# Kernel tuning notes

Measured on AMD Instinct MI355X. Metric: run time of the kernel, lower is better.

## Reference

```python
import jax, jax.numpy as jnp
import numpy as np

N_NODES = 50000
N_EDGES = 800000
HIDDEN = 64
NUM_FEATURES = 1
OUT_DIM = 2


def setup_inputs() -> dict:
    key = jax.random.key(0)
    k = jax.random.split(key, 6)
    x = jax.random.normal(k[0], (N_NODES, NUM_FEATURES), dtype=jnp.float32)
    edge_index = jax.random.randint(k[1], (2, N_EDGES), 0, N_NODES, dtype=jnp.int32)
    # GCNConv params (PyG default: glorot weight, zero bias; random here for testing)
    W1 = jax.random.normal(k[2], (NUM_FEATURES, HIDDEN), dtype=jnp.float32) * 0.5
    b1 = jax.random.normal(k[3], (HIDDEN,), dtype=jnp.float32) * 0.1
    W2 = jax.random.normal(k[4], (HIDDEN, OUT_DIM), dtype=jnp.float32) * 0.1
    b2 = jax.random.normal(k[5], (OUT_DIM,), dtype=jnp.float32) * 0.1
    return {"x": x, "edge_index": edge_index, "W1": W1, "b1": b1, "W2": W2, "b2": b2}


def _gcn_norm(edge_index, num_nodes):
    # PyG gcn_norm with add_self_loops=True, symmetric normalization
    row, col = edge_index[0], edge_index[1]
    loop = jnp.arange(num_nodes, dtype=row.dtype)
    row = jnp.concatenate([row, loop])
    col = jnp.concatenate([col, loop])
    ew = jnp.ones(row.shape[0], dtype=jnp.float32)
    deg = jax.ops.segment_sum(ew, col, num_segments=num_nodes)  # in-degree incl. self-loop
    dinv = jnp.where(deg > 0, jax.lax.rsqrt(deg), 0.0)
    norm = dinv[row] * dinv[col]  # [E+N]
    return row, col, norm


def _gcn_conv(x, row, col, norm, W, b, num_nodes):
    h = x @ W                                  # [N, out] transform first (out <= in here is fine)
    msg = h[row] * norm[:, None]               # gather + scale, [E+N, out]
    out = jax.ops.segment_sum(msg, col, num_segments=num_nodes)  # scatter-add at targets
    return out + b


def reference(x, edge_index, W1, b1, W2, b2):
    row, col, norm = _gcn_norm(edge_index, N_NODES)
    h = _gcn_conv(x, row, col, norm, W1, b1, N_NODES)
    h = jax.nn.relu(h)
    out = _gcn_conv(h, row, col, norm, W2, b2, N_NODES)
    return out
```

## Files before the change

### kernel.cpp

```cpp
#include <hip/hip_runtime.h>
#include <math.h>

#define N_NODES 50000
#define N_EDGES 800000
#define HIDDEN  64
#define NPART   500
#define PCHUNK  1600
#define NBUCK   32
#define SLICE   1568
#define CAPB    128
#define NSUB    10
#define BPS     (NPART / NSUB)
#define SPAN    (BPS * CAPB)


__global__ __launch_bounds__(256)
void k_part(const int* __restrict__ row, const int* __restrict__ col,
            unsigned* __restrict__ cnts, unsigned* __restrict__ bks) {
    __shared__ unsigned stage[NBUCK * CAPB];
    __shared__ unsigned cnt2[NBUCK];
    const int t   = threadIdx.x;
    const int blk = blockIdx.x;
    const int e0  = blk * PCHUNK;
    if (t < NBUCK) cnt2[t] = 0u;
    __syncthreads();
    const int4* c4 = (const int4*)(col + e0);
    const int4* r4 = (const int4*)(row + e0);
    for (int i = t; i < PCHUNK / 4; i += 256) {
        int4 cv = c4[i];
        int4 rv = r4[i];
#pragma unroll
        for (int k = 0; k < 4; ++k) {
            int c = (&cv.x)[k], r = (&rv.x)[k];
            int b = c / SLICE;
            unsigned off = atomicAdd(&cnt2[b], 1u);
            if (off < CAPB)
                stage[(b << 7) + off] = ((unsigned)(c - b * SLICE) << 16) | (unsigned)r;
        }
    }
    __syncthreads();
    if (t < NBUCK) cnts[blk * NBUCK + t] = min(cnt2[t], (unsigned)CAPB);
    for (int i = t; i < NBUCK * CAPB; i += 256) {
        int b = i >> 7, o = i & 127;
        bks[((size_t)b * NPART + blk) * CAPB + o] = stage[i];
    }
}

__global__ __launch_bounds__(256)
void k_deg(const unsigned* __restrict__ cnts, const unsigned* __restrict__ bks,
           unsigned* __restrict__ part_deg) {
    __shared__ unsigned acc[SLICE];
    __shared__ unsigned short scnt[BPS];
    const int b = blockIdx.x / NSUB;
    const int s = blockIdx.x % NSUB;
    for (int i = threadIdx.x; i < SLICE; i += 256) acc[i] = 0u;
    if (threadIdx.x < BPS)
        scnt[threadIdx.x] = (unsigned short)cnts[(s * BPS + threadIdx.x) * NBUCK + b];
    __syncthreads();
    const unsigned* src = bks + ((size_t)b * NPART + s * BPS) * CAPB;
    for (int i = threadIdx.x; i < SPAN; i += 256) {
        unsigned v = src[i];
        if ((unsigned)(i & 127) < scnt[i >> 7]) atomicAdd(&acc[v >> 16], 1u);
    }
    __syncthreads();
    unsigned* dst = part_deg + (size_t)blockIdx.x * SLICE;
    for (int i = threadIdx.x; i < SLICE; i += 256) dst[i] = acc[i];
}

__global__ __launch_bounds__(256)
void k_g(const unsigned* __restrict__ part_deg, const float* __restrict__ x,
         float* __restrict__ dinv, float* __restrict__ g) {
    int n = blockIdx.x * 256 + threadIdx.x;
    if (n >= N_NODES) return;
    int b = n / SLICE, cl = n - b * SLICE;
    const unsigned* p = part_deg + (size_t)b * NSUB * SLICE + cl;
    unsigned deg = 0;
#pragma unroll
    for (int s = 0; s < NSUB; ++s) deg += p[(size_t)s * SLICE];
    float di = rsqrtf((float)(deg + 1));
    dinv[n] = di;
    g[n] = di * x[n];
}

__global__ __launch_bounds__(256)
void k_agg1(const unsigned* __restrict__ cnts, const unsigned* __restrict__ bks,
            const float* __restrict__ g, float* __restrict__ part1) {
    __shared__ float acc[SLICE];
    __shared__ unsigned short scnt[BPS];
    const int b = blockIdx.x / NSUB;
    const int s = blockIdx.x % NSUB;
    for (int i = threadIdx.x; i < SLICE; i += 256) acc[i] = 0.0f;
    if (threadIdx.x < BPS)
        scnt[threadIdx.x] = (unsigned short)cnts[(s * BPS + threadIdx.x) * NBUCK + b];
    __syncthreads();
    const unsigned* src = bks + ((size_t)b * NPART + s * BPS) * CAPB;
    for (int i = threadIdx.x; i < SPAN; i += 256) {
        unsigned v = src[i];
        if ((unsigned)(i & 127) < scnt[i >> 7])
            atomicAdd(&acc[v >> 16], g[v & 0xFFFFu]);
    }
    __syncthreads();
    float* dst = part1 + (size_t)blockIdx.x * SLICE;
    for (int i = threadIdx.x; i < SLICE; i += 256) dst[i] = acc[i];
}

__global__ __launch_bounds__(256)
void k_mlp(const float* __restrict__ part1, const float* __restrict__ g,
           const float* __restrict__ dinv,
           const float* __restrict__ W1, const float* __restrict__ b1,
           const float* __restrict__ W2, float2* __restrict__ z) {
    int n = blockIdx.x * 256 + threadIdx.x;
    if (n >= N_NODES) return;
    int b = n / SLICE, cl = n - b * SLICE;
    const float* p = part1 + (size_t)b * NSUB * SLICE + cl;
    float t = 0.0f;
#pragma unroll
    for (int s = 0; s < NSUB; ++s) t += p[(size_t)s * SLICE];
    float di = dinv[n];
    float sv = di * (t + g[n]);
    float y0 = 0.0f, y1 = 0.0f;
#pragma unroll
    for (int k = 0; k < HIDDEN; ++k) {
        float h = fmaxf(sv * W1[k] + b1[k], 0.0f);
        y0 += h * W2[2 * k];
        y1 += h * W2[2 * k + 1];
    }
    z[n] = make_float2(di * y0, di * y1);
}

__global__ __launch_bounds__(256)
void k_agg2(const unsigned* __restrict__ cnts, const unsigned* __restrict__ bks,
            const float2* __restrict__ z, float2* __restrict__ part2) {
    __shared__ float ax[SLICE];
    __shared__ float ay[SLICE];
    __shared__ unsigned short scnt[BPS];
    const int b = blockIdx.x / NSUB;
    const int s = blockIdx.x % NSUB;
    for (int i = threadIdx.x; i < SLICE; i += 256) { ax[i] = 0.0f; ay[i] = 0.0f; }
    if (threadIdx.x < BPS)
        scnt[threadIdx.x] = (unsigned short)cnts[(s * BPS + threadIdx.x) * NBUCK + b];
    __syncthreads();
    const unsigned* src = bks + ((size_t)b * NPART + s * BPS) * CAPB;
    for (int i = threadIdx.x; i < SPAN; i += 256) {
        unsigned v = src[i];
        if ((unsigned)(i & 127) < scnt[i >> 7]) {
            float2 zz = z[v & 0xFFFFu];
            unsigned cl = v >> 16;
            atomicAdd(&ax[cl], zz.x);
            atomicAdd(&ay[cl], zz.y);
        }
    }
    __syncthreads();
    float2* dst = part2 + (size_t)blockIdx.x * SLICE;
    for (int i = threadIdx.x; i < SLICE; i += 256) dst[i] = make_float2(ax[i], ay[i]);
}

__global__ __launch_bounds__(256)
void k_final(const float2* __restrict__ part2, const float2* __restrict__ z,
             const float* __restrict__ dinv, const float* __restrict__ b2,
             float2* __restrict__ out) {
    int n = blockIdx.x * 256 + threadIdx.x;
    if (n >= N_NODES) return;
    int b = n / SLICE, cl = n - b * SLICE;
    const float2* p = part2 + (size_t)b * NSUB * SLICE + cl;
    float Tx = 0.0f, Ty = 0.0f;
#pragma unroll
    for (int s = 0; s < NSUB; ++s) {
        float2 v = p[(size_t)s * SLICE];
        Tx += v.x; Ty += v.y;
    }
    float di = dinv[n];
    float2 zn = z[n];
    out[n] = make_float2(di * (Tx + zn.x) + b2[0], di * (Ty + zn.y) + b2[1]);
}


extern "C" void kernel_launch(void* const* d_in, const int* in_sizes, int n_in,
                              void* d_out, int out_size, void* d_ws, size_t ws_size,
                              hipStream_t stream) {
    const float* x  = (const float*)d_in[0];
    const int*   ei = (const int*)d_in[1];
    const float* W1 = (const float*)d_in[2];
    const float* b1 = (const float*)d_in[3];
    const float* W2 = (const float*)d_in[4];
    const float* b2 = (const float*)d_in[5];

    const int* row = ei;
    const int* col = ei + N_EDGES;

    char* p = (char*)d_ws;
    unsigned* cnts     = (unsigned*)p;  p += (size_t)NPART * NBUCK * 4;
    unsigned* bks      = (unsigned*)p;  p += (size_t)NBUCK * NPART * CAPB * 4;
    unsigned* part_deg = (unsigned*)p;  p += (size_t)NBUCK * NSUB * SLICE * 4;
    float*    part1    = (float*)p;     p += (size_t)NBUCK * NSUB * SLICE * 4;
    float2*   part2    = (float2*)p;    p += (size_t)NBUCK * NSUB * SLICE * 8;
    float*    dinv     = (float*)p;     p += N_NODES * 4;
    float*    g        = (float*)p;     p += N_NODES * 4;
    float2*   z        = (float2*)p;

    const int gA = NBUCK * NSUB;
    const int gN = (N_NODES + 255) / 256;

    k_part <<<NPART, 256, 0, stream>>>(row, col, cnts, bks);
    k_deg  <<<gA,    256, 0, stream>>>(cnts, bks, part_deg);
    k_g    <<<gN,    256, 0, stream>>>(part_deg, x, dinv, g);
    k_agg1 <<<gA,    256, 0, stream>>>(cnts, bks, g, part1);
    k_mlp  <<<gN,    256, 0, stream>>>(part1, g, dinv, W1, b1, W2, z);
    k_agg2 <<<gA,    256, 0, stream>>>(cnts, bks, z, part2);
    k_final<<<gN,    256, 0, stream>>>(part2, z, dinv, b2, (float2*)d_out);
}
```

Before: 123.2 us.

## Compact edge buckets with global atomic tails instead of padded per-partition slots

The partition kernel now reserves space in each destination bucket with a global atomicAdd on a per-bucket tail and writes only valid entries contiguously. The aggregation kernels then stream a dense contiguous range split into NSUB=8 chunks, no longer scanning padded 128-slot blocks with per-slot validity checks. This removes reading padding (about 2x the real edges) in three aggregation passes and uses fewer blocks. In exchange it adds a memset launch and global atomics, and the edge order within a bucket becomes nondeterministic, which changes floating-point summation order.

```diff
diff --git a/kernel.cpp b/kernel.cpp
--- a/kernel.cpp
+++ b/kernel.cpp
@@ -9,16 +9,15 @@
 #define NBUCK   32
 #define SLICE   1568
 #define CAPB    128
-#define NSUB    10
-#define BPS     (NPART / NSUB)
-#define SPAN    (BPS * CAPB)
+#define BCAP    26000
+#define NSUB    8
 
 
 __global__ __launch_bounds__(256)
 void k_part(const int* __restrict__ row, const int* __restrict__ col,
-            unsigned* __restrict__ cnts, unsigned* __restrict__ bks) {
+            unsigned* __restrict__ tails, unsigned* __restrict__ bks) {
     __shared__ unsigned stage[NBUCK * CAPB];
-    __shared__ unsigned cnt2[NBUCK];
+    __shared__ unsigned cnt2[NBUCK], gpos[NBUCK];
     const int t   = threadIdx.x;
     const int blk = blockIdx.x;
     const int e0  = blk * PCHUNK;
@@ -39,29 +38,35 @@
         }
     }
     __syncthreads();
-    if (t < NBUCK) cnts[blk * NBUCK + t] = min(cnt2[t], (unsigned)CAPB);
+    if (t < NBUCK) {
+        unsigned cc = min(cnt2[t], (unsigned)CAPB);
+        cnt2[t] = cc;
+        gpos[t] = atomicAdd(&tails[t], cc);
+    }
+    __syncthreads();
     for (int i = t; i < NBUCK * CAPB; i += 256) {
-        int b = i >> 7, o = i & 127;
-        bks[((size_t)b * NPART + blk) * CAPB + o] = stage[i];
-    }
-}
-
-__global__ __launch_bounds__(256)
-void k_deg(const unsigned* __restrict__ cnts, const unsigned* __restrict__ bks,
+        int b = i >> 7; unsigned o = (unsigned)(i & 127);
+        if (o < cnt2[b]) {
+            unsigned dst = gpos[b] + o;
+            if (dst < BCAP) bks[(size_t)b * BCAP + dst] = stage[i];
+        }
+    }
+}
+
+__global__ __launch_bounds__(256)
+void k_deg(const unsigned* __restrict__ tails, const unsigned* __restrict__ bks,
            unsigned* __restrict__ part_deg) {
     __shared__ unsigned acc[SLICE];
-    __shared__ unsigned short scnt[BPS];
-    const int b = blockIdx.x / NSUB;
-    const int s = blockIdx.x % NSUB;
+    const int b = blockIdx.x >> 3;
+    const int s = blockIdx.x & (NSUB - 1);
     for (int i = threadIdx.x; i < SLICE; i += 256) acc[i] = 0u;
-    if (threadIdx.x < BPS)
-        scnt[threadIdx.x] = (unsigned short)cnts[(s * BPS + threadIdx.x) * NBUCK + b];
-    __syncthreads();
-    const unsigned* src = bks + ((size_t)b * NPART + s * BPS) * CAPB;
-    for (int i = threadIdx.x; i < SPAN; i += 256) {
-        unsigned v = src[i];
-        if ((unsigned)(i & 127) < scnt[i >> 7]) atomicAdd(&acc[v >> 16], 1u);
-    }
+    __syncthreads();
+    unsigned tail = min(tails[b], (unsigned)BCAP);
+    unsigned chunk = (tail + NSUB - 1) / NSUB;
+    unsigned lo = s * chunk, hi = min(lo + chunk, tail);
+    const unsigned* bk = bks + (size_t)b * BCAP;
+    for (unsigned i = lo + threadIdx.x; i < hi; i += 256)
+        atomicAdd(&acc[bk[i] >> 16], 1u);
     __syncthreads();
     unsigned* dst = part_deg + (size_t)blockIdx.x * SLICE;
     for (int i = threadIdx.x; i < SLICE; i += 256) dst[i] = acc[i];
@@ -83,21 +88,20 @@
 }
 
 __global__ __launch_bounds__(256)
-void k_agg1(const unsigned* __restrict__ cnts, const unsigned* __restrict__ bks,
+void k_agg1(const unsigned* __restrict__ tails, const unsigned* __restrict__ bks,
             const float* __restrict__ g, float* __restrict__ part1) {
     __shared__ float acc[SLICE];
-    __shared__ unsigned short scnt[BPS];
-    const int b = blockIdx.x / NSUB;
-    const int s = blockIdx.x % NSUB;
+    const int b = blockIdx.x >> 3;
+    const int s = blockIdx.x & (NSUB - 1);
     for (int i = threadIdx.x; i < SLICE; i += 256) acc[i] = 0.0f;
-    if (threadIdx.x < BPS)
-        scnt[threadIdx.x] = (unsigned short)cnts[(s * BPS + threadIdx.x) * NBUCK + b];
-    __syncthreads();
-    const unsigned* src = bks + ((size_t)b * NPART + s * BPS) * CAPB;
-    for (int i = threadIdx.x; i < SPAN; i += 256) {
-        unsigned v = src[i];
-        if ((unsigned)(i & 127) < scnt[i >> 7])
-            atomicAdd(&acc[v >> 16], g[v & 0xFFFFu]);
+    __syncthreads();
+    unsigned tail = min(tails[b], (unsigned)BCAP);
+    unsigned chunk = (tail + NSUB - 1) / NSUB;
+    unsigned lo = s * chunk, hi = min(lo + chunk, tail);
+    const unsigned* bk = bks + (size_t)b * BCAP;
+    for (unsigned i = lo + threadIdx.x; i < hi; i += 256) {
+        unsigned v = bk[i];
+        atomicAdd(&acc[v >> 16], g[v & 0xFFFFu]);
     }
     __syncthreads();
     float* dst = part1 + (size_t)blockIdx.x * SLICE;
@@ -129,26 +133,24 @@
 }
 
 __global__ __launch_bounds__(256)
-void k_agg2(const unsigned* __restrict__ cnts, const unsigned* __restrict__ bks,
+void k_agg2(const unsigned* __restrict__ tails, const unsigned* __restrict__ bks,
             const float2* __restrict__ z, float2* __restrict__ part2) {
     __shared__ float ax[SLICE];
     __shared__ float ay[SLICE];
-    __shared__ unsigned short scnt[BPS];
-    const int b = blockIdx.x / NSUB;
-    const int s = blockIdx.x % NSUB;
+    const int b = blockIdx.x >> 3;
+    const int s = blockIdx.x & (NSUB - 1);
     for (int i = threadIdx.x; i < SLICE; i += 256) { ax[i] = 0.0f; ay[i] = 0.0f; }
-    if (threadIdx.x < BPS)
-        scnt[threadIdx.x] = (unsigned short)cnts[(s * BPS + threadIdx.x) * NBUCK + b];
-    __syncthreads();
-    const unsigned* src = bks + ((size_t)b * NPART + s * BPS) * CAPB;
-    for (int i = threadIdx.x; i < SPAN; i += 256) {
-        unsigned v = src[i];
-        if ((unsigned)(i & 127) < scnt[i >> 7]) {
-            float2 zz = z[v & 0xFFFFu];
-            unsigned cl = v >> 16;
-            atomicAdd(&ax[cl], zz.x);
-            atomicAdd(&ay[cl], zz.y);
-        }
+    __syncthreads();
+    unsigned tail = min(tails[b], (unsigned)BCAP);
+    unsigned chunk = (tail + NSUB - 1) / NSUB;
+    unsigned lo = s * chunk, hi = min(lo + chunk, tail);
+    const unsigned* bk = bks + (size_t)b * BCAP;
+    for (unsigned i = lo + threadIdx.x; i < hi; i += 256) {
+        unsigned v = bk[i];
+        float2 zz = z[v & 0xFFFFu];
+        unsigned cl = v >> 16;
+        atomicAdd(&ax[cl], zz.x);
+        atomicAdd(&ay[cl], zz.y);
     }
     __syncthreads();
     float2* dst = part2 + (size_t)blockIdx.x * SLICE;
@@ -189,8 +191,8 @@
     const int* col = ei + N_EDGES;
 
     char* p = (char*)d_ws;
-    unsigned* cnts     = (unsigned*)p;  p += (size_t)NPART * NBUCK * 4;
-    unsigned* bks      = (unsigned*)p;  p += (size_t)NBUCK * NPART * CAPB * 4;
+    unsigned* tails    = (unsigned*)p;  p += 128;
+    unsigned* bks      = (unsigned*)p;  p += (size_t)NBUCK * BCAP * 4;
     unsigned* part_deg = (unsigned*)p;  p += (size_t)NBUCK * NSUB * SLICE * 4;
     float*    part1    = (float*)p;     p += (size_t)NBUCK * NSUB * SLICE * 4;
     float2*   part2    = (float2*)p;    p += (size_t)NBUCK * NSUB * SLICE * 8;
@@ -201,11 +203,12 @@
     const int gA = NBUCK * NSUB;
     const int gN = (N_NODES + 255) / 256;
 
-    k_part <<<NPART, 256, 0, stream>>>(row, col, cnts, bks);
-    k_deg  <<<gA,    256, 0, stream>>>(cnts, bks, part_deg);
+    hipMemsetAsync(tails, 0, NBUCK * sizeof(unsigned), stream);
+    k_part <<<NPART, 256, 0, stream>>>(row, col, tails, bks);
+    k_deg  <<<gA,    256, 0, stream>>>(tails, bks, part_deg);
     k_g    <<<gN,    256, 0, stream>>>(part_deg, x, dinv, g);
-    k_agg1 <<<gA,    256, 0, stream>>>(cnts, bks, g, part1);
+    k_agg1 <<<gA,    256, 0, stream>>>(tails, bks, g, part1);
     k_mlp  <<<gN,    256, 0, stream>>>(part1, g, dinv, W1, b1, W2, z);
-    k_agg2 <<<gA,    256, 0, stream>>>(cnts, bks, z, part2);
+    k_agg2 <<<gA,    256, 0, stream>>>(tails, bks, z, part2);
     k_final<<<gN,    256, 0, stream>>>(part2, z, dinv, b2, (float2*)d_out);
 }
```

Result: faster. 112.8 us (median of 2 runs) (-8.4%).
